# Optimization experiments

Hardware: AMD Instinct MI355X
Metric: run time of the kernel (lower is better)

Reference implementation:

```python
import jax, jax.numpy as jnp
import numpy as np

SEQ_LEN, BATCH, HID, EMB, VOCAB = 80, 5120, 256, 8, 100


def lstm_layer(xs, w_ih, w_hh, b_ih, b_hh):
    # xs: [T, B, in]; PyTorch gate order i, f, g, o
    B = xs.shape[1]
    H = w_hh.shape[1]
    x_proj = jnp.einsum('tbi,gi->tbg', xs, w_ih) + b_ih + b_hh  # [T, B, 4H]

    def step(carry, xp_t):
        h, c = carry
        gates = xp_t + h @ w_hh.T
        i, f, g, o = jnp.split(gates, 4, axis=-1)
        c = jax.nn.sigmoid(f) * c + jax.nn.sigmoid(i) * jnp.tanh(g)
        h = jax.nn.sigmoid(o) * jnp.tanh(c)
        return (h, c), h

    init = (jnp.zeros((B, H), xs.dtype), jnp.zeros((B, H), xs.dtype))
    (h_n, c_n), ys = jax.lax.scan(step, init, x_proj)
    return ys, h_n


def setup_inputs() -> dict:
    key = jax.random.key(0)
    ks = jax.random.split(key, 12)
    s_h = 1.0 / np.sqrt(HID)
    inp = {
        'x': jax.random.randint(ks[0], (SEQ_LEN, BATCH), 0, VOCAB),
        'emb': jax.random.normal(ks[1], (VOCAB, EMB), jnp.float32),
        'w_ih0': jax.random.uniform(ks[2], (4 * HID, EMB), jnp.float32, -s_h, s_h),
        'w_hh0': jax.random.uniform(ks[3], (4 * HID, HID), jnp.float32, -s_h, s_h),
        'b_ih0': jax.random.uniform(ks[4], (4 * HID,), jnp.float32, -s_h, s_h),
        'b_hh0': jax.random.uniform(ks[5], (4 * HID,), jnp.float32, -s_h, s_h),
        'w_ih1': jax.random.uniform(ks[6], (4 * HID, HID), jnp.float32, -s_h, s_h),
        'w_hh1': jax.random.uniform(ks[7], (4 * HID, HID), jnp.float32, -s_h, s_h),
        'b_ih1': jax.random.uniform(ks[8], (4 * HID,), jnp.float32, -s_h, s_h),
        'b_hh1': jax.random.uniform(ks[9], (4 * HID,), jnp.float32, -s_h, s_h),
        'dec_w': jax.random.uniform(ks[10], (VOCAB, HID * SEQ_LEN), jnp.float32, -0.01, 0.01),
        'dec_b': jax.random.uniform(ks[11], (VOCAB,), jnp.float32, -0.01, 0.01),
    }
    return inp


def reference(x, emb, w_ih0, w_hh0, b_ih0, b_hh0, w_ih1, w_hh1, b_ih1, b_hh1, dec_w, dec_b):
    encoded = emb[x]                                   # [T, B, EMB]
    ys0, _ = lstm_layer(encoded, w_ih0, w_hh0, b_ih0, b_hh0)  # [T, B, H]
    ys1, _ = lstm_layer(ys0, w_ih1, w_hh1, b_ih1, b_hh1)      # [T, B, H]
    last = ys1[-1]                                     # [B, H] (last timestep)
    # faithful to original quirk: view(-1, hidden*seq_len) -> [B/seq_len, H*T]
    flat = last.reshape(-1, HID * SEQ_LEN)
    return flat @ dec_w.T + dec_b                      # [B/seq_len, VOCAB]
```

## Files before the change

### kernel.cpp

```cpp
#include <hip/hip_runtime.h>

#define T_SEQ 80
#define NB    5120
#define NBH   (NB * 256)
#define NVOC  100

#define OFF_TABLE0 0u
#define OFF_BIAS1  409600u
#define OFF_BPACK  413696u
#define OFF_RING0  1986560u
#define OFF_RING1  7229440u
#define OFF_C0     12472320u
#define OFF_C1     15093760u

#define SMEM_BYTES 42624

typedef float  f32x4  __attribute__((ext_vector_type(4)));
typedef __bf16 bf16x8 __attribute__((ext_vector_type(8)));
typedef short  s16x8  __attribute__((ext_vector_type(8)));
typedef _Float16 f16x4 __attribute__((ext_vector_type(4)));
typedef unsigned short u16x8 __attribute__((ext_vector_type(8)));

__device__ __forceinline__ int colmap(int np) {
  int gate = (np >> 4) & 3;
  int j    = ((np >> 6) << 4) | (np & 15);
  return gate * 256 + j;
}

__device__ __forceinline__ unsigned short f2bf(float f) {
  unsigned int u = __float_as_uint(f);
  u += 0x7fffu + ((u >> 16) & 1u);
  return (unsigned short)(u >> 16);
}
__device__ __forceinline__ float bf2f(unsigned short s) {
  return __uint_as_float(((unsigned int)s) << 16);
}
__device__ __forceinline__ float sigm(float x) {
  x = fminf(fmaxf(x, -20.f), 20.f);
  return 1.f / (1.f + __expf(-x));
}
__device__ __forceinline__ float tanh_(float x) {
  x = fminf(fmaxf(x, -10.f), 10.f);
  float e = __expf(2.f * x);
  return (e - 1.f) / (e + 1.f);
}

__global__ void prep_kernel(const float* __restrict__ emb,
                            const float* __restrict__ w_ih0, const float* __restrict__ w_hh0,
                            const float* __restrict__ b_ih0, const float* __restrict__ b_hh0,
                            const float* __restrict__ w_ih1, const float* __restrict__ w_hh1,
                            const float* __restrict__ b_ih1, const float* __restrict__ b_hh1,
                            float* __restrict__ table0, float* __restrict__ bias1,
                            unsigned short* __restrict__ Bpack) {
  int idx = blockIdx.x * 256 + threadIdx.x;
  if (idx < 102400) {
    int v = idx >> 10, np = idx & 1023;
    int row = colmap(np);
    float s = b_ih0[row] + b_hh0[row];
#pragma unroll
    for (int e = 0; e < 8; ++e) s = fmaf(emb[v * 8 + e], w_ih0[row * 8 + e], s);
    table0[idx] = s;
  } else if (idx < 103424) {
    int np = idx - 102400;
    bias1[np] = b_ih1[colmap(np)] + b_hh1[colmap(np)];
  } else {
    int i2 = idx - 103424;
    int i    = i2 & 7;
    int t    = (i2 >> 3) & 511;
    int ni   = (i2 >> 12) & 7;
    int slot = i2 >> 15;
    int np   = ni * 128 + ((t >> 6) << 4) + (t & 15);
    int row  = colmap(np);
    int k    = (((t & 63) >> 4) << 3) + i;
    float val;
    if (slot < 8) {
      val = w_hh0[row * 256 + slot * 32 + k];
    } else {
      int kc = slot - 8;
      const float* W = (kc < 8) ? w_ih1 : w_hh1;
      val = W[row * 256 + (kc & 7) * 32 + k];
    }
    Bpack[i2] = f2bf(val);
  }
}

__global__ __launch_bounds__(256, 1) void step_kernel(
    int s, const int* __restrict__ x,
    const float* __restrict__ table0, const float* __restrict__ bias1,
    const unsigned short* __restrict__ Bpack,
    unsigned short* __restrict__ ring0, unsigned short* __restrict__ ring1,
    _Float16* __restrict__ c0h, _Float16* __restrict__ c1h) {
  extern __shared__ char smem[];
  char* Ab = smem;
  char* Bb = smem + 25600;
  int*  xs = (int*)(smem + 41984);

  const int tid = threadIdx.x;
  const int lane = tid & 63, wid = tid >> 6;
  const int l15 = lane & 15, lhi = lane >> 4;
  const int wm = wid >> 1, wn = wid & 1, rw = wm * 80;

  const int p = blockIdx.x;
  const int xcd = p & 7, idx = p >> 3;
  const bool isL0 = idx < 32;
  const int sub = idx & 31;
  const int mi = xcd * 4 + (sub >> 3);
  const int ni = sub & 7;
  const int rows = mi * 160;

  int t;
  if (isL0) { if (s == T_SEQ) return; t = s; }
  else      { if (s == 0)     return; t = s - 1; }

  const unsigned short* ring0Prev = ring0 + ((s + 1) & 1) * NBH;
  unsigned short*       ring0Cur  = ring0 + (s & 1) * NBH;
  const unsigned short* h1Prev    = ring1 + (s & 1) * NBH;
  unsigned short*       h1Cur     = ring1 + ((s + 1) & 1) * NBH;

  const int KC = isL0 ? (t > 0 ? 8 : 0) : (t > 0 ? 16 : 8);

  if (isL0 && tid < 160) xs[tid] = x[t * NB + rows + tid];

  f32x4 acc[5][4];
#pragma unroll
  for (int m = 0; m < 5; ++m)
#pragma unroll
    for (int nf = 0; nf < 4; ++nf) acc[m][nf] = (f32x4)0.f;

  uint4 au0, au1, au2;
  s16x8 bsr0, bsr1;

#define LOADR(kc_) do { \
    const unsigned short* _As; int _ko; \
    if (isL0) { _As = ring0Prev; _ko = (kc_) * 32; } \
    else { _As = ((kc_) < 8) ? ring0Prev : h1Prev; _ko = ((kc_) & 7) * 32; } \
    { int _c = tid;       au0 = *(const uint4*)(_As + (rows + (_c >> 2)) * 256 + _ko + ((_c & 3) << 3)); } \
    { int _c = tid + 256; au1 = *(const uint4*)(_As + (rows + (_c >> 2)) * 256 + _ko + ((_c & 3) << 3)); } \
    if (tid < 128) { int _c = tid + 512; au2 = *(const uint4*)(_As + (rows + (_c >> 2)) * 256 + _ko + ((_c & 3) << 3)); } \
    int _slot = isL0 ? (kc_) : (8 + (kc_)); \
    bsr0 = *(const s16x8*)(Bpack + (((_slot * 8 + ni) * 512 + tid) << 3)); \
    bsr1 = *(const s16x8*)(Bpack + (((_slot * 8 + ni) * 512 + tid + 256) << 3)); \
  } while (0)

#define STORER(buf_) do { \
    char* _ab = Ab + (buf_) * 12800; \
    *(uint4*)(_ab + (tid >> 2) * 80 + (tid & 3) * 16) = au0; \
    { int _c = tid + 256; *(uint4*)(_ab + (_c >> 2) * 80 + (_c & 3) * 16) = au1; } \
    if (tid < 128) { int _c = tid + 512; *(uint4*)(_ab + (_c >> 2) * 80 + (_c & 3) * 16) = au2; } \
    char* _bb = Bb + (buf_) * 8192; \
    *(s16x8*)(_bb + tid * 16) = bsr0; \
    *(s16x8*)(_bb + (tid + 256) * 16) = bsr1; \
  } while (0)

#define CONSUME(buf_) do { \
    const char* _ab = Ab + (buf_) * 12800; \
    const char* _bp = Bb + (buf_) * 8192; \
    bf16x8 _bld[4]; \
    _Pragma("unroll") \
    for (int _nf = 0; _nf < 4; ++_nf) \
      _bld[_nf] = *(const bf16x8*)(_bp + ((wn * 4 + _nf) * 64 + lane) * 16); \
    _Pragma("unroll") \
    for (int _m = 0; _m < 5; ++_m) { \
      bf16x8 _a = *(const bf16x8*)(_ab + (rw + _m * 16 + l15) * 80 + lhi * 16); \
      _Pragma("unroll") \
      for (int _nf = 0; _nf < 4; ++_nf) \
        acc[_m][_nf] = __builtin_amdgcn_mfma_f32_16x16x32_bf16(_a, _bld[_nf], acc[_m][_nf], 0, 0, 0); \
    } \
  } while (0)

  if (KC > 0) { LOADR(0); STORER(0); }
#pragma unroll 1
  for (int kc = 0; kc < KC; ++kc) {
    __syncthreads();
    const bool more = (kc + 1 < KC);
    if (more) LOADR(kc + 1);
    CONSUME(kc & 1);
    if (more) STORER((kc + 1) & 1);
  }
  if (KC == 0) __syncthreads();

  const int jh = (ni * 2 + wn) * 16 + l15;
  if (isL0) {
    const int tbb = ni * 128 + wn * 64 + l15;
#pragma unroll
    for (int m = 0; m < 5; ++m) {
      const int cbase = ((rows + rw + m * 16) >> 2) + lhi;
      f16x4 cold4 = (f16x4)(_Float16)0.f;
      if (t > 0) cold4 = *(const f16x4*)(c0h + cbase * 1024 + jh * 4);
      f16x4 cnew;
#pragma unroll
      for (int r = 0; r < 4; ++r) {
        int rowl = rw + m * 16 + lhi * 4 + r;
        const float* tb = table0 + xs[rowl] * 1024 + tbb;
        float gi = acc[m][0][r] + tb[0];
        float gf = acc[m][1][r] + tb[16];
        float gg = acc[m][2][r] + tb[32];
        float go = acc[m][3][r] + tb[48];
        float cn = sigm(gf) * (float)cold4[r] + sigm(gi) * tanh_(gg);
        cnew[r] = (_Float16)cn;
        ring0Cur[(rows + rowl) * 256 + jh] = f2bf(sigm(go) * tanh_(cn));
      }
      *(f16x4*)(c0h + cbase * 1024 + jh * 4) = cnew;
    }
  } else {
    const int bbb = ni * 128 + wn * 64 + l15;
    float b0 = bias1[bbb], b1 = bias1[bbb + 16], b2 = bias1[bbb + 32], b3 = bias1[bbb + 48];
#pragma unroll
    for (int m = 0; m < 5; ++m) {
      const int cbase = ((rows + rw + m * 16) >> 2) + lhi;
      f16x4 cold4 = (f16x4)(_Float16)0.f;
      if (t > 0) cold4 = *(const f16x4*)(c1h + cbase * 1024 + jh * 4);
      f16x4 cnew;
#pragma unroll
      for (int r = 0; r < 4; ++r) {
        int rowl = rw + m * 16 + lhi * 4 + r;
        float gi = acc[m][0][r] + b0;
        float gf = acc[m][1][r] + b1;
        float gg = acc[m][2][r] + b2;
        float go = acc[m][3][r] + b3;
        float cn = sigm(gf) * (float)cold4[r] + sigm(gi) * tanh_(gg);
        cnew[r] = (_Float16)cn;
        h1Cur[(rows + rowl) * 256 + jh] = f2bf(sigm(go) * tanh_(cn));
      }
      *(f16x4*)(c1h + cbase * 1024 + jh * 4) = cnew;
    }
  }
#undef LOADR
#undef STORER
#undef CONSUME
}

__global__ __launch_bounds__(256) void decoder_kernel(
    const unsigned short* __restrict__ h1, const float* __restrict__ dec_w,
    const float* __restrict__ dec_b, float* __restrict__ out) {
  __shared__ float hs[5120];
  const int tid = threadIdx.x, lane = tid & 63, wid = tid >> 6;
  const int b = blockIdx.x;
  const int r = b >> 2;
  const int qoff = (b & 3) * 5120;

  const unsigned short* src = h1 + (size_t)b * 5120;
  for (int i = tid; i < 640; i += 256) {
    u16x8 v8 = *(const u16x8*)(src + i * 8);
#pragma unroll
    for (int e = 0; e < 8; ++e) hs[i * 8 + e] = bf2f(v8[e]);
  }
  __syncthreads();

  for (int vv = wid; vv < NVOC; vv += 4) {
    const float* wp = dec_w + (size_t)vv * 20480 + qoff + lane * 4;
    const float* hp = hs + lane * 4;
    float s = 0.f;
#pragma unroll
    for (int it = 0; it < 20; ++it) {
      f32x4 w4 = *(const f32x4*)(wp + it * 256);
      f32x4 h4 = *(const f32x4*)(hp + it * 256);
      s += w4[0] * h4[0] + w4[1] * h4[1] + w4[2] * h4[2] + w4[3] * h4[3];
    }
#pragma unroll
    for (int off = 32; off > 0; off >>= 1) s += __shfl_down(s, off, 64);
    if (lane == 0) {
      if ((b & 3) == 0) s += dec_b[vv];
      atomicAdd(&out[r * 100 + vv], s);
    }
  }
}

extern "C" void kernel_launch(void* const* d_in, const int* in_sizes, int n_in,
                              void* d_out, int out_size, void* d_ws, size_t ws_size,
                              hipStream_t stream) {
  const int*   x     = (const int*)d_in[0];
  const float* emb   = (const float*)d_in[1];
  const float* w_ih0 = (const float*)d_in[2];
  const float* w_hh0 = (const float*)d_in[3];
  const float* b_ih0 = (const float*)d_in[4];
  const float* b_hh0 = (const float*)d_in[5];
  const float* w_ih1 = (const float*)d_in[6];
  const float* w_hh1 = (const float*)d_in[7];
  const float* b_ih1 = (const float*)d_in[8];
  const float* b_hh1 = (const float*)d_in[9];
  const float* dec_w = (const float*)d_in[10];
  const float* dec_b = (const float*)d_in[11];
  float* out = (float*)d_out;
  char* ws = (char*)d_ws;

  float*          table0 = (float*)(ws + OFF_TABLE0);
  float*          bias1  = (float*)(ws + OFF_BIAS1);
  unsigned short* Bpack  = (unsigned short*)(ws + OFF_BPACK);
  unsigned short* ring0  = (unsigned short*)(ws + OFF_RING0);
  unsigned short* ring1  = (unsigned short*)(ws + OFF_RING1);
  _Float16*       c0h    = (_Float16*)(ws + OFF_C0);
  _Float16*       c1h    = (_Float16*)(ws + OFF_C1);

  hipMemsetAsync(out, 0, (size_t)out_size * 4, stream);
  prep_kernel<<<3476, 256, 0, stream>>>(emb, w_ih0, w_hh0, b_ih0, b_hh0,
                                        w_ih1, w_hh1, b_ih1, b_hh1,
                                        table0, bias1, Bpack);
  hipFuncSetAttribute((const void*)step_kernel,
                      hipFuncAttributeMaxDynamicSharedMemorySize, SMEM_BYTES);
  for (int s = 0; s <= T_SEQ; ++s)
    step_kernel<<<512, 256, SMEM_BYTES, stream>>>(s, x, table0, bias1, Bpack,
                                                  ring0, ring1, c0h, c1h);
  decoder_kernel<<<256, 256, 0, stream>>>(ring1 + NBH, dec_w, dec_b, out);
}
```

Baseline: 1.523 ms.

## Fold output zeroing into prep, prefetch cell state early, batch decoder rows

```diff
diff --git a/kernel.cpp b/kernel.cpp
--- a/kernel.cpp
+++ b/kernel.cpp
@@ -51,8 +51,10 @@
                             const float* __restrict__ w_ih1, const float* __restrict__ w_hh1,
                             const float* __restrict__ b_ih1, const float* __restrict__ b_hh1,
                             float* __restrict__ table0, float* __restrict__ bias1,
-                            unsigned short* __restrict__ Bpack) {
+                            unsigned short* __restrict__ Bpack,
+                            float* __restrict__ out, int out_size) {
   int idx = blockIdx.x * 256 + threadIdx.x;
+  if (idx < out_size) out[idx] = 0.f;
   if (idx < 102400) {
     int v = idx >> 10, np = idx & 1023;
     int row = colmap(np);
@@ -118,8 +120,26 @@
   unsigned short*       h1Cur     = ring1 + ((s + 1) & 1) * NBH;
 
   const int KC = isL0 ? (t > 0 ? 8 : 0) : (t > 0 ? 16 : 8);
+  const int jh = (ni * 2 + wn) * 16 + l15;
 
   if (isL0 && tid < 160) xs[tid] = x[t * NB + rows + tid];
+
+  _Float16* ch = isL0 ? c0h : c1h;
+  f16x4 cold[5];
+#pragma unroll
+  for (int m = 0; m < 5; ++m) cold[m] = (f16x4)(_Float16)0.f;
+  if (t > 0) {
+#pragma unroll
+    for (int m = 0; m < 5; ++m) {
+      const int cbase = ((rows + rw + m * 16) >> 2) + lhi;
+      cold[m] = *(const f16x4*)(ch + cbase * 1024 + jh * 4);
+    }
+  }
+  float b0 = 0.f, b1 = 0.f, b2 = 0.f, b3 = 0.f;
+  if (!isL0) {
+    const int bbb = ni * 128 + wn * 64 + l15;
+    b0 = bias1[bbb]; b1 = bias1[bbb + 16]; b2 = bias1[bbb + 32]; b3 = bias1[bbb + 48];
+  }
 
   f32x4 acc[5][4];
 #pragma unroll
@@ -179,14 +199,11 @@
   }
   if (KC == 0) __syncthreads();
 
-  const int jh = (ni * 2 + wn) * 16 + l15;
   if (isL0) {
     const int tbb = ni * 128 + wn * 64 + l15;
 #pragma unroll
     for (int m = 0; m < 5; ++m) {
       const int cbase = ((rows + rw + m * 16) >> 2) + lhi;
-      f16x4 cold4 = (f16x4)(_Float16)0.f;
-      if (t > 0) cold4 = *(const f16x4*)(c0h + cbase * 1024 + jh * 4);
       f16x4 cnew;
 #pragma unroll
       for (int r = 0; r < 4; ++r) {
@@ -196,20 +213,16 @@
         float gf = acc[m][1][r] + tb[16];
         float gg = acc[m][2][r] + tb[32];
         float go = acc[m][3][r] + tb[48];
-        float cn = sigm(gf) * (float)cold4[r] + sigm(gi) * tanh_(gg);
+        float cn = sigm(gf) * (float)cold[m][r] + sigm(gi) * tanh_(gg);
         cnew[r] = (_Float16)cn;
         ring0Cur[(rows + rowl) * 256 + jh] = f2bf(sigm(go) * tanh_(cn));
       }
       *(f16x4*)(c0h + cbase * 1024 + jh * 4) = cnew;
     }
   } else {
-    const int bbb = ni * 128 + wn * 64 + l15;
-    float b0 = bias1[bbb], b1 = bias1[bbb + 16], b2 = bias1[bbb + 32], b3 = bias1[bbb + 48];
 #pragma unroll
     for (int m = 0; m < 5; ++m) {
       const int cbase = ((rows + rw + m * 16) >> 2) + lhi;
-      f16x4 cold4 = (f16x4)(_Float16)0.f;
-      if (t > 0) cold4 = *(const f16x4*)(c1h + cbase * 1024 + jh * 4);
       f16x4 cnew;
 #pragma unroll
       for (int r = 0; r < 4; ++r) {
@@ -218,7 +231,7 @@
         float gf = acc[m][1][r] + b1;
         float gg = acc[m][2][r] + b2;
         float go = acc[m][3][r] + b3;
-        float cn = sigm(gf) * (float)cold4[r] + sigm(gi) * tanh_(gg);
+        float cn = sigm(gf) * (float)cold[m][r] + sigm(gi) * tanh_(gg);
         cnew[r] = (_Float16)cn;
         h1Cur[(rows + rowl) * 256 + jh] = f2bf(sigm(go) * tanh_(cn));
       }
@@ -233,35 +246,56 @@
 __global__ __launch_bounds__(256) void decoder_kernel(
     const unsigned short* __restrict__ h1, const float* __restrict__ dec_w,
     const float* __restrict__ dec_b, float* __restrict__ out) {
-  __shared__ float hs[5120];
+  __shared__ float hs[4][2560];
   const int tid = threadIdx.x, lane = tid & 63, wid = tid >> 6;
   const int b = blockIdx.x;
-  const int r = b >> 2;
-  const int qoff = (b & 3) * 5120;
-
-  const unsigned short* src = h1 + (size_t)b * 5120;
-  for (int i = tid; i < 640; i += 256) {
-    u16x8 v8 = *(const u16x8*)(src + i * 8);
-#pragma unroll
-    for (int e = 0; e < 8; ++e) hs[i * 8 + e] = bf2f(v8[e]);
+  const int win = b & 7;
+  const int rt  = b >> 3;
+  const int qoff = win * 2560;
+
+#pragma unroll
+  for (int rr = 0; rr < 4; ++rr) {
+    const unsigned short* src = h1 + (size_t)(rt * 4 + rr) * 20480 + qoff;
+    for (int i = tid; i < 320; i += 256) {
+      u16x8 v8 = *(const u16x8*)(src + i * 8);
+#pragma unroll
+      for (int e = 0; e < 8; ++e) hs[rr][i * 8 + e] = bf2f(v8[e]);
+    }
   }
   __syncthreads();
 
   for (int vv = wid; vv < NVOC; vv += 4) {
     const float* wp = dec_w + (size_t)vv * 20480 + qoff + lane * 4;
-    const float* hp = hs + lane * 4;
-    float s = 0.f;
-#pragma unroll
-    for (int it = 0; it < 20; ++it) {
+    float s0 = 0.f, s1 = 0.f, s2 = 0.f, s3 = 0.f;
+#pragma unroll
+    for (int it = 0; it < 10; ++it) {
       f32x4 w4 = *(const f32x4*)(wp + it * 256);
-      f32x4 h4 = *(const f32x4*)(hp + it * 256);
-      s += w4[0] * h4[0] + w4[1] * h4[1] + w4[2] * h4[2] + w4[3] * h4[3];
-    }
-#pragma unroll
-    for (int off = 32; off > 0; off >>= 1) s += __shfl_down(s, off, 64);
+      const int qq = it * 256 + lane * 4;
+      f32x4 h0 = *(const f32x4*)&hs[0][qq];
+      f32x4 h1v = *(const f32x4*)&hs[1][qq];
+      f32x4 h2 = *(const f32x4*)&hs[2][qq];
+      f32x4 h3 = *(const f32x4*)&hs[3][qq];
+#pragma unroll
+      for (int e = 0; e < 4; ++e) {
+        s0 = fmaf(w4[e], h0[e], s0);
+        s1 = fmaf(w4[e], h1v[e], s1);
+        s2 = fmaf(w4[e], h2[e], s2);
+        s3 = fmaf(w4[e], h3[e], s3);
+      }
+    }
+#pragma unroll
+    for (int off = 32; off > 0; off >>= 1) {
+      s0 += __shfl_down(s0, off, 64);
+      s1 += __shfl_down(s1, off, 64);
+      s2 += __shfl_down(s2, off, 64);
+      s3 += __shfl_down(s3, off, 64);
+    }
     if (lane == 0) {
-      if ((b & 3) == 0) s += dec_b[vv];
-      atomicAdd(&out[r * 100 + vv], s);
+      float bias = (win == 0) ? dec_b[vv] : 0.f;
+      atomicAdd(&out[(rt * 4 + 0) * 100 + vv], s0 + bias);
+      atomicAdd(&out[(rt * 4 + 1) * 100 + vv], s1 + bias);
+      atomicAdd(&out[(rt * 4 + 2) * 100 + vv], s2 + bias);
+      atomicAdd(&out[(rt * 4 + 3) * 100 + vv], s3 + bias);
     }
   }
 }
@@ -292,14 +326,13 @@
   _Float16*       c0h    = (_Float16*)(ws + OFF_C0);
   _Float16*       c1h    = (_Float16*)(ws + OFF_C1);
 
-  hipMemsetAsync(out, 0, (size_t)out_size * 4, stream);
   prep_kernel<<<3476, 256, 0, stream>>>(emb, w_ih0, w_hh0, b_ih0, b_hh0,
                                         w_ih1, w_hh1, b_ih1, b_hh1,
-                                        table0, bias1, Bpack);
+                                        table0, bias1, Bpack, out, out_size);
   hipFuncSetAttribute((const void*)step_kernel,
                       hipFuncAttributeMaxDynamicSharedMemorySize, SMEM_BYTES);
   for (int s = 0; s <= T_SEQ; ++s)
     step_kernel<<<512, 256, SMEM_BYTES, stream>>>(s, x, table0, bias1, Bpack,
                                                   ring0, ring1, c0h, c1h);
-  decoder_kernel<<<256, 256, 0, stream>>>(ring1 + NBH, dec_w, dec_b, out);
-}
+  decoder_kernel<<<128, 256, 0, stream>>>(ring1 + NBH, dec_w, dec_b, out);
+}
```

After: 1.487 ms. 2.3% less time.
